# Performance work log

Measured on AMD Instinct MI355X. Metric: run time of the kernel, lower is better.

Reference implementation:

```python
import jax, jax.numpy as jnp
import numpy as np

B, S, D, H, L, FFN = 32, 512, 512, 8, 4, 1024
DH = D // H
EPS = 1e-5


def make_pe(seq, d):
    pos = np.arange(seq)[:, None].astype(np.float64)
    i = np.arange(d)[None, :]
    angle = pos / np.power(10000.0, (i // 2 * 2.0) / d)
    pe = angle.copy()
    pe[:, 0::2] = np.sin(angle[:, 0::2])
    pe[:, 1::2] = np.cos(angle[:, 1::2])
    return jnp.asarray(pe, dtype=jnp.float32)


def layer_norm(x, g, b):
    mu = jnp.mean(x, axis=-1, keepdims=True)
    var = jnp.mean((x - mu) ** 2, axis=-1, keepdims=True)
    return (x - mu) * jax.lax.rsqrt(var + EPS) * g + b


def setup_inputs() -> dict:
    key = jax.random.key(0)
    ks = jax.random.split(key, 12)
    sd = 0.02
    d = {
        "x": jax.random.normal(ks[0], (B, S, D), dtype=jnp.float32),
        "pe": make_pe(S, D),
        "Wq": jax.random.normal(ks[1], (L, D, D), dtype=jnp.float32) * sd,
        "bq": jnp.zeros((L, D), dtype=jnp.float32),
        "Wk": jax.random.normal(ks[2], (L, D, D), dtype=jnp.float32) * sd,
        "bk": jnp.zeros((L, D), dtype=jnp.float32),
        "Wv": jax.random.normal(ks[3], (L, D, D), dtype=jnp.float32) * sd,
        "bv": jnp.zeros((L, D), dtype=jnp.float32),
        "Wo": jax.random.normal(ks[4], (L, D, D), dtype=jnp.float32) * sd,
        "bo": jnp.zeros((L, D), dtype=jnp.float32),
        "ln1_g": jnp.ones((L, D), dtype=jnp.float32),
        "ln1_b": jnp.zeros((L, D), dtype=jnp.float32),
        "W1": jax.random.normal(ks[5], (L, D, FFN), dtype=jnp.float32) * sd,
        "b1": jnp.zeros((L, FFN), dtype=jnp.float32),
        "W2": jax.random.normal(ks[6], (L, FFN, D), dtype=jnp.float32) * sd,
        "b2": jnp.zeros((L, D), dtype=jnp.float32),
        "ln2_g": jnp.ones((L, D), dtype=jnp.float32),
        "ln2_b": jnp.zeros((L, D), dtype=jnp.float32),
    }
    return d


def reference(x, pe, Wq, bq, Wk, bk, Wv, bv, Wo, bo, ln1_g, ln1_b,
              W1, b1, W2, b2, ln2_g, ln2_b):
    out = x + pe  # positional encoding (dropout = identity in eval)
    scale = DH ** (-0.5)
    for l in range(L):
        # projections (B,S,D)
        Q = out @ Wq[l] + bq[l]
        K = out @ Wk[l] + bk[l]
        V = out @ Wv[l] + bv[l]
        # faithful raw view (no head transpose), matching torch .view semantics
        Qh = Q.reshape(B * H, S, DH)
        Kh = K.reshape(B * H, S, DH)
        Vh = V.reshape(B * H, S, DH)
        att = jnp.einsum('bqd,bkd->bqk', Qh, Kh) * scale  # (B*H,S,S)
        att = jax.nn.softmax(att, axis=-1)
        ctx = jnp.einsum('bqk,bkd->bqd', att, Vh).reshape(B, S, D)
        a = layer_norm(ctx @ Wo[l] + bo[l] + out, ln1_g[l], ln1_b[l])
        # position-wise FFN
        h = jax.nn.relu(a @ W1[l] + b1[l])
        out = layer_norm(h @ W2[l] + b2[l] + a, ln2_g[l], ln2_b[l])
    return out.reshape(B, S * D)
```

## Files before the change

### kernel.cpp

```cpp
#include <hip/hip_runtime.h>
#include <stdint.h>

#define NB 32
#define NS 512
#define ND 512
#define NH 8
#define NL 4
#define NF 1024
#define NDH 64
#define NM (NB*NS)
#define WLSTRIDE 2097152

typedef __attribute__((ext_vector_type(8))) short bf16x8;
typedef __attribute__((ext_vector_type(4))) float f32x4;

__device__ __forceinline__ short f2bf(float f) {
    union { float f; uint32_t u; } v; v.f = f;
    uint32_t r = (v.u + 0x7FFFu + ((v.u >> 16) & 1u)) >> 16;
    return (short)r;
}
__device__ __forceinline__ float bf2f(short s) {
    union { uint32_t u; float f; } v; v.u = ((uint32_t)(uint16_t)s) << 16;
    return v.f;
}
__device__ __forceinline__ f32x4 mfma16(bf16x8 a, bf16x8 b, f32x4 c) {
    return __builtin_amdgcn_mfma_f32_16x16x32_bf16(a, b, c, 0, 0, 0);
}
__device__ __forceinline__ void gld16(const void* g, void* l) {
    __builtin_amdgcn_global_load_lds(
        (const __attribute__((address_space(1))) void*)g,
        (__attribute__((address_space(3))) void*)l, 16, 0, 0);
}
__device__ __forceinline__ void xcd_swz(int& bx, int& by, int gx, int gy) {
    int n = gx * gy;
    int f = by * gx + bx;
    int q = n >> 3;
    int xcd = f & 7, idx = f >> 3;
    int s = xcd * q + idx;
    bx = s % gx; by = s / gx;
}

__global__ __launch_bounds__(256) void convT_k(const float* __restrict__ src,
        short* __restrict__ dst, int K, int N, int woff, int total)
{
    int i = blockIdx.x * 256 + threadIdx.x;
    if (i >= total) return;
    int per = K * N;
    int l = i / per, r = i - l * per;
    int n = r / K, k = r - n * K;
    dst[(size_t)l * WLSTRIDE + woff + r] = f2bf(src[(size_t)l * per + (size_t)k * N + n]);
}

__global__ __launch_bounds__(256) void biaspack_k(const float* __restrict__ bq,
        const float* __restrict__ bk, const float* __restrict__ bv, float* __restrict__ out)
{
    int i = blockIdx.x * 256 + threadIdx.x;
    if (i >= NL * 1536) return;
    int l = i / 1536, j = i - l * 1536;
    float v = (j < 512) ? bq[l * 512 + j] : (j < 1024) ? bk[l * 512 + j - 512]
                                                       : bv[l * 512 + j - 1024];
    out[i] = v;
}

__global__ __launch_bounds__(256) void addpe_k(const float* __restrict__ x,
        const float* __restrict__ pe, short* __restrict__ X)
{
    size_t i = ((size_t)blockIdx.x * 256 + threadIdx.x) * 8;
    size_t sd = i % (size_t)(NS * ND);
    f32x4 a0 = *(const f32x4*)(x + i);
    f32x4 a1 = *(const f32x4*)(x + i + 4);
    f32x4 p0 = *(const f32x4*)(pe + sd);
    f32x4 p1 = *(const f32x4*)(pe + sd + 4);
    bf16x8 r;
    #pragma unroll
    for (int j = 0; j < 4; j++) { r[j] = f2bf(a0[j] + p0[j]); r[4 + j] = f2bf(a1[j] + p1[j]); }
    *(bf16x8*)(X + i) = r;
}

template<int EPI>
__global__ __launch_bounds__(256) void gemm_bt(
        const short* __restrict__ A, const short* __restrict__ Bt,
        const float* __restrict__ bias, const short* __restrict__ res,
        void* __restrict__ C0, void* __restrict__ C1, void* __restrict__ C2,
        int M, int N, int K)
{
    __shared__ __align__(16) short Al[8192];
    __shared__ __align__(16) short Bl[8192];
    const int tid = threadIdx.x;
    const int wid = tid >> 6, lane = tid & 63;
    int bx = blockIdx.x, by = blockIdx.y;
    xcd_swz(bx, by, gridDim.x, gridDim.y);
    const int m0 = by * 128, n0 = bx * 128;
    const int wr = wid >> 1, wc = wid & 1;

    f32x4 acc[4][4];
    f32x4 zz = {0.f, 0.f, 0.f, 0.f};
    #pragma unroll
    for (int i = 0; i < 4; i++)
        #pragma unroll
        for (int j = 0; j < 4; j++) acc[i][j] = zz;

    const size_t rk = (size_t)K * 2;
    const char* Ab = (const char*)A + (size_t)m0 * rk;
    const char* Bb = (const char*)Bt + (size_t)n0 * rk;

    int srow[4], scol[4];
    #pragma unroll
    for (int c = 0; c < 4; c++) {
        int p = c * 4096 + tid * 16;
        int l = p ^ (((p >> 7) & 7) << 4);
        srow[c] = l >> 7;  scol[c] = l & 127;
    }

    for (int k0 = 0; k0 < K; k0 += 64) {
        __syncthreads();
        #pragma unroll
        for (int c = 0; c < 4; c++)
            gld16(Ab + (size_t)srow[c] * rk + (size_t)k0 * 2 + scol[c],
                  (char*)Al + c * 4096 + wid * 1024);
        #pragma unroll
        for (int c = 0; c < 4; c++)
            gld16(Bb + (size_t)srow[c] * rk + (size_t)k0 * 2 + scol[c],
                  (char*)Bl + c * 4096 + wid * 1024);
        __syncthreads();
        #pragma unroll
        for (int ks = 0; ks < 2; ks++) {
            bf16x8 af[4], bfr[4];
            #pragma unroll
            for (int mf = 0; mf < 4; mf++) {
                int row = wr * 64 + mf * 16 + (lane & 15);
                int off = (row * 128 + ks * 64 + ((lane >> 4) * 16)) ^ ((row & 7) << 4);
                af[mf] = *(const bf16x8*)((const char*)Al + off);
            }
            #pragma unroll
            for (int nf = 0; nf < 4; nf++) {
                int row = wc * 64 + nf * 16 + (lane & 15);
                int off = (row * 128 + ks * 64 + ((lane >> 4) * 16)) ^ ((row & 7) << 4);
                bfr[nf] = *(const bf16x8*)((const char*)Bl + off);
            }
            #pragma unroll
            for (int mf = 0; mf < 4; mf++)
                #pragma unroll
                for (int nf = 0; nf < 4; nf++)
                    acc[mf][nf] = mfma16(af[mf], bfr[nf], acc[mf][nf]);
        }
    }

    void* outp;
    int colbase, ostride;
    if (EPI == 0) {
        int seg = n0 >> 9;
        outp = (seg == 0) ? C0 : (seg == 1) ? C1 : C2;
        colbase = n0 & 511; ostride = 512;
    } else {
        outp = C0; colbase = n0; ostride = N;
    }

    #pragma unroll
    for (int mf = 0; mf < 4; mf++) {
        #pragma unroll
        for (int nf = 0; nf < 4; nf++) {
            int colg = n0 + wc * 64 + nf * 16 + (lane & 15);
            int col  = colbase + wc * 64 + nf * 16 + (lane & 15);
            float bi = bias[colg];
            #pragma unroll
            for (int r = 0; r < 4; r++) {
                int row = m0 + wr * 64 + mf * 16 + ((lane >> 4) << 2) + r;
                float v = acc[mf][nf][r] + bi;
                if (EPI == 0) {
                    ((short*)outp)[(size_t)row * 512 + col] = f2bf(v);
                } else if (EPI == 1) {
                    ((short*)outp)[(size_t)row * ostride + col] = f2bf(fmaxf(v, 0.f));
                } else {
                    v += bf2f(res[(size_t)row * ostride + col]);
                    ((float*)outp)[(size_t)row * ostride + col] = v;
                }
            }
        }
    }
}

__global__ __launch_bounds__(256) void vtrans_k(const short* __restrict__ V,
        short* __restrict__ VT)
{
    __shared__ short T[64][65];
    const int tid = threadIdx.x;
    const int r0 = blockIdx.x * 64, g = blockIdx.y;
    const size_t base = (size_t)g * 32768;
    #pragma unroll
    for (int rep = 0; rep < 2; rep++) {
        int chunk = rep * 256 + tid;
        int sr = chunk >> 3, c8 = (chunk & 7) * 8;
        bf16x8 v = *(const bf16x8*)(V + base + (size_t)(r0 + sr) * 64 + c8);
        #pragma unroll
        for (int j = 0; j < 8; j++) T[sr][c8 + j] = v[j];
    }
    __syncthreads();
    #pragma unroll
    for (int rep = 0; rep < 2; rep++) {
        int chunk = rep * 256 + tid;
        int dh = chunk >> 3, c8 = (chunk & 7) * 8;
        bf16x8 w;
        #pragma unroll
        for (int j = 0; j < 8; j++) w[j] = T[c8 + j][dh];
        *(bf16x8*)(VT + base + (size_t)dh * 512 + r0 + c8) = w;
    }
}

__global__ __launch_bounds__(256) void attn_k(
        const short* __restrict__ Q, const short* __restrict__ Kb,
        const short* __restrict__ VT, short* __restrict__ ctx)
{
    __shared__ __align__(16) short Kl[4096];
    __shared__ __align__(16) short Vl[4096];
    __shared__ __align__(16) short Pl[8192];
    const int tid = threadIdx.x, wid = tid >> 6, lane = tid & 63;
    int bx = blockIdx.x, by = blockIdx.y;
    xcd_swz(bx, by, gridDim.x, gridDim.y);
    const int g = by, q0 = bx * 128;
    const size_t base = (size_t)g * 32768;
    const float C = 0.18033688f;

    bf16x8 qa[2][2];
    #pragma unroll
    for (int qf = 0; qf < 2; qf++)
        #pragma unroll
        for (int ks = 0; ks < 2; ks++)
            qa[qf][ks] = *(const bf16x8*)(Q + base
                + (size_t)(q0 + wid * 32 + qf * 16 + (lane & 15)) * 64
                + ks * 32 + ((lane >> 4) * 8));

    f32x4 o[2][4];
    float ps[2][4];
    f32x4 zz = {0.f, 0.f, 0.f, 0.f};
    #pragma unroll
    for (int qf = 0; qf < 2; qf++) {
        #pragma unroll
        for (int nf = 0; nf < 4; nf++) o[qf][nf] = zz;
        #pragma unroll
        for (int r = 0; r < 4; r++) ps[qf][r] = 0.f;
    }

    const char* Kbase = (const char*)(Kb + base);
    const char* Vbase = (const char*)(VT + base);

    int srow[2], scol[2];
    #pragma unroll
    for (int c = 0; c < 2; c++) {
        int p = c * 4096 + tid * 16;
        int l = p ^ (((p >> 7) & 7) << 4);
        srow[c] = l >> 7;  scol[c] = l & 127;
    }

    for (int kt = 0; kt < 8; kt++) {
        __syncthreads();
        #pragma unroll
        for (int c = 0; c < 2; c++) {
            int p = c * 4096 + tid * 16;
            int sp = p ^ (((p >> 7) & 7) << 4);
            gld16(Kbase + (size_t)kt * 8192 + sp, (char*)Kl + c * 4096 + wid * 1024);
        }
        #pragma unroll
        for (int c = 0; c < 2; c++)
            gld16(Vbase + (size_t)srow[c] * 1024 + kt * 128 + scol[c],
                  (char*)Vl + c * 4096 + wid * 1024);
        __syncthreads();

        f32x4 sc[2][4];
        #pragma unroll
        for (int qf = 0; qf < 2; qf++)
            #pragma unroll
            for (int nf = 0; nf < 4; nf++) sc[qf][nf] = zz;
        #pragma unroll
        for (int ks = 0; ks < 2; ks++) {
            #pragma unroll
            for (int nf = 0; nf < 4; nf++) {
                int kvr = nf * 16 + (lane & 15);
                int bo = (kvr * 128 + ks * 64 + ((lane >> 4) * 16)) ^ ((kvr & 7) << 4);
                bf16x8 kf = *(const bf16x8*)((const char*)Kl + bo);
                #pragma unroll
                for (int qf = 0; qf < 2; qf++)
                    sc[qf][nf] = mfma16(qa[qf][ks], kf, sc[qf][nf]);
            }
        }

        #pragma unroll
        for (int qf = 0; qf < 2; qf++) {
            #pragma unroll
            for (int r = 0; r < 4; r++) {
                int qr = wid * 32 + qf * 16 + ((lane >> 4) << 2) + r;
                float s4 = 0.f;
                #pragma unroll
                for (int nf = 0; nf < 4; nf++) {
                    float p = __builtin_amdgcn_exp2f(sc[qf][nf][r] * C);
                    s4 += p;
                    int bo = (qr * 128 + (nf * 16 + (lane & 15)) * 2) ^ ((qr & 7) << 4);
                    *(short*)((char*)Pl + bo) = f2bf(p);
                }
                ps[qf][r] += s4;
            }
        }

        #pragma unroll
        for (int ks = 0; ks < 2; ks++) {
            bf16x8 pa[2];
            #pragma unroll
            for (int qf = 0; qf < 2; qf++) {
                int qrb = wid * 32 + qf * 16 + (lane & 15);
                int bo = (qrb * 128 + ks * 64 + ((lane >> 4) * 16)) ^ ((qrb & 7) << 4);
                pa[qf] = *(const bf16x8*)((const char*)Pl + bo);
            }
            #pragma unroll
            for (int nf = 0; nf < 4; nf++) {
                int dh = nf * 16 + (lane & 15);
                int bo2 = (dh * 128 + ks * 64 + ((lane >> 4) * 16)) ^ ((dh & 7) << 4);
                bf16x8 vf = *(const bf16x8*)((const char*)Vl + bo2);
                #pragma unroll
                for (int qf = 0; qf < 2; qf++)
                    o[qf][nf] = mfma16(pa[qf], vf, o[qf][nf]);
            }
        }
    }

    #pragma unroll
    for (int qf = 0; qf < 2; qf++) {
        #pragma unroll
        for (int r = 0; r < 4; r++) {
            float s = ps[qf][r];
            s += __shfl_xor(s, 1);
            s += __shfl_xor(s, 2);
            s += __shfl_xor(s, 4);
            s += __shfl_xor(s, 8);
            float inv = 1.f / s;
            int qr = q0 + wid * 32 + qf * 16 + ((lane >> 4) << 2) + r;
            #pragma unroll
            for (int nf = 0; nf < 4; nf++) {
                int dh = nf * 16 + (lane & 15);
                ctx[base + (size_t)qr * 64 + dh] = f2bf(o[qf][nf][r] * inv);
            }
        }
    }
}

template<int OUTF32>
__global__ __launch_bounds__(256) void ln_k(
        const float* __restrict__ pre, const float* __restrict__ g,
        const float* __restrict__ b, void* __restrict__ out)
{
    int row = blockIdx.x * 4 + (threadIdx.x >> 6);
    int lane = threadIdx.x & 63;
    const float* x = pre + (size_t)row * ND + lane * 8;
    f32x4 a0 = *(const f32x4*)x;
    f32x4 a1 = *(const f32x4*)(x + 4);
    float s = 0.f, sq = 0.f;
    #pragma unroll
    for (int j = 0; j < 4; j++) { s += a0[j]; sq += a0[j] * a0[j]; s += a1[j]; sq += a1[j] * a1[j]; }
    #pragma unroll
    for (int d = 1; d < 64; d <<= 1) { s += __shfl_xor(s, d); sq += __shfl_xor(sq, d); }
    float mean = s * (1.f / ND);
    float var = sq * (1.f / ND) - mean * mean;
    float rstd = rsqrtf(var + 1e-5f);
    const float* gp = g + lane * 8;
    const float* bp = b + lane * 8;
    if (OUTF32) {
        float* op = (float*)out + (size_t)row * ND + lane * 8;
        f32x4 r0, r1;
        #pragma unroll
        for (int j = 0; j < 4; j++) {
            r0[j] = (a0[j] - mean) * rstd * gp[j] + bp[j];
            r1[j] = (a1[j] - mean) * rstd * gp[4 + j] + bp[4 + j];
        }
        *(f32x4*)op = r0;
        *(f32x4*)(op + 4) = r1;
    } else {
        bf16x8 rr;
        #pragma unroll
        for (int j = 0; j < 4; j++) {
            rr[j]     = f2bf((a0[j] - mean) * rstd * gp[j] + bp[j]);
            rr[4 + j] = f2bf((a1[j] - mean) * rstd * gp[4 + j] + bp[4 + j]);
        }
        *(bf16x8*)((short*)out + (size_t)row * ND + lane * 8) = rr;
    }
}

extern "C" void kernel_launch(void* const* d_in, const int* in_sizes, int n_in,
                              void* d_out, int out_size, void* d_ws, size_t ws_size,
                              hipStream_t stream)
{
    (void)in_sizes; (void)n_in; (void)out_size; (void)ws_size;
    const float* x   = (const float*)d_in[0];
    const float* pe  = (const float*)d_in[1];
    const float* Wq  = (const float*)d_in[2];
    const float* bq  = (const float*)d_in[3];
    const float* Wk  = (const float*)d_in[4];
    const float* bk  = (const float*)d_in[5];
    const float* Wv  = (const float*)d_in[6];
    const float* bv  = (const float*)d_in[7];
    const float* Wo  = (const float*)d_in[8];
    const float* bo  = (const float*)d_in[9];
    const float* g1  = (const float*)d_in[10];
    const float* be1 = (const float*)d_in[11];
    const float* W1  = (const float*)d_in[12];
    const float* b1  = (const float*)d_in[13];
    const float* W2  = (const float*)d_in[14];
    const float* b2  = (const float*)d_in[15];
    const float* g2  = (const float*)d_in[16];
    const float* be2 = (const float*)d_in[17];

    char* ws = (char*)d_ws;
    const size_t MB = 1048576;
    short* WT   = (short*)(ws);
    short* XB   = (short*)(ws + 16 * MB);
    short* QB   = (short*)(ws + 32 * MB);
    short* KB   = (short*)(ws + 48 * MB);
    short* VB   = (short*)(ws + 64 * MB);
    short* VTb  = (short*)(ws + 80 * MB);
    short* CT   = (short*)(ws + 96 * MB);
    float* BQKV = (float*)(ws + 112 * MB);
    short* AB   = QB;
    float* PR   = (float*)KB;
    short* HB   = VTb;

    convT_k<<<dim3((NL*ND*ND + 255) / 256), 256, 0, stream>>>(Wq, WT, ND, ND, 0,       NL*ND*ND);
    convT_k<<<dim3((NL*ND*ND + 255) / 256), 256, 0, stream>>>(Wk, WT, ND, ND, 262144,  NL*ND*ND);
    convT_k<<<dim3((NL*ND*ND + 255) / 256), 256, 0, stream>>>(Wv, WT, ND, ND, 524288,  NL*ND*ND);
    convT_k<<<dim3((NL*ND*ND + 255) / 256), 256, 0, stream>>>(Wo, WT, ND, ND, 786432,  NL*ND*ND);
    convT_k<<<dim3((NL*ND*NF + 255) / 256), 256, 0, stream>>>(W1, WT, ND, NF, 1048576, NL*ND*NF);
    convT_k<<<dim3((NL*NF*ND + 255) / 256), 256, 0, stream>>>(W2, WT, NF, ND, 1572864, NL*NF*ND);
    biaspack_k<<<dim3(24), 256, 0, stream>>>(bq, bk, bv, BQKV);

    addpe_k<<<dim3(4096), 256, 0, stream>>>(x, pe, XB);

    for (int l = 0; l < NL; l++) {
        const short* wl = WT + (size_t)l * WLSTRIDE;
        gemm_bt<0><<<dim3(12, 128), 256, 0, stream>>>(XB, wl, BQKV + l*1536, nullptr,
                                                      QB, KB, VB, NM, 1536, ND);
        vtrans_k<<<dim3(8, 256), 256, 0, stream>>>(VB, VTb);
        attn_k<<<dim3(4, 256), 256, 0, stream>>>(QB, KB, VTb, CT);
        gemm_bt<2><<<dim3(4, 128), 256, 0, stream>>>(CT, wl + 786432, bo + l*ND, XB,
                                                     PR, nullptr, nullptr, NM, ND, ND);
        ln_k<0><<<dim3(4096), 256, 0, stream>>>(PR, g1 + l*ND, be1 + l*ND, AB);
        gemm_bt<1><<<dim3(8, 128), 256, 0, stream>>>(AB, wl + 1048576, b1 + l*NF, nullptr,
                                                     HB, nullptr, nullptr, NM, NF, ND);
        gemm_bt<2><<<dim3(4, 128), 256, 0, stream>>>(HB, wl + 1572864, b2 + l*ND, AB,
                                                     PR, nullptr, nullptr, NM, ND, NF);
        if (l < NL - 1)
            ln_k<0><<<dim3(4096), 256, 0, stream>>>(PR, g2 + l*ND, be2 + l*ND, XB);
        else
            ln_k<1><<<dim3(4096), 256, 0, stream>>>(PR, g2 + l*ND, be2 + l*ND, (float*)d_out);
    }
}
```

Measured before the change: 908.1 us.

## Double-buffer LDS tiles in GEMM and attention; tile the weight transpose

The GEMM and attention kernels now keep two shared-memory buffers and issue the global-to-LDS loads for the next K tile while the current tile is being computed. Waits use explicit vmcnt counts and barriers in place of the earlier per-iteration syncthreads, so load latency is meant to hide behind MFMA work. The weight conversion/transpose kernel becomes a 64x64 LDS-tiled transpose with coalesced reads and writes. The cost is twice the LDS per block, which can lower occupancy, and the hand-written waitcnt and barrier scheme depends on each thread issuing a fixed number of loads.

Result: faster. 780.6 us (-14.0%).

```diff
diff --git a/kernel.cpp b/kernel.cpp
--- a/kernel.cpp
+++ b/kernel.cpp
@@ -12,7 +12,14 @@
 #define WLSTRIDE 2097152
 
 typedef __attribute__((ext_vector_type(8))) short bf16x8;
+typedef __attribute__((ext_vector_type(4))) short s16x4;
 typedef __attribute__((ext_vector_type(4))) float f32x4;
+
+#define VM0  asm volatile("s_waitcnt vmcnt(0)" ::: "memory")
+#define VM4  asm volatile("s_waitcnt vmcnt(4)" ::: "memory")
+#define VM8  asm volatile("s_waitcnt vmcnt(8)" ::: "memory")
+#define SCHB __builtin_amdgcn_sched_barrier(0)
+#define SB   __builtin_amdgcn_s_barrier()
 
 __device__ __forceinline__ short f2bf(float f) {
     union { float f; uint32_t u; } v; v.f = f;
@@ -41,14 +48,32 @@
 }
 
 __global__ __launch_bounds__(256) void convT_k(const float* __restrict__ src,
-        short* __restrict__ dst, int K, int N, int woff, int total)
-{
-    int i = blockIdx.x * 256 + threadIdx.x;
-    if (i >= total) return;
-    int per = K * N;
-    int l = i / per, r = i - l * per;
-    int n = r / K, k = r - n * K;
-    dst[(size_t)l * WLSTRIDE + woff + r] = f2bf(src[(size_t)l * per + (size_t)k * N + n]);
+        short* __restrict__ dst, int K, int N, int woff)
+{
+    __shared__ float T[64][65];
+    int tk = K >> 6, tn = N >> 6;
+    int bid = blockIdx.x;
+    int l = bid / (tk * tn), rb = bid % (tk * tn);
+    int k0 = (rb / tn) << 6, n0 = (rb % tn) << 6;
+    const float* s = src + (size_t)l * K * N;
+    short* d = dst + (size_t)l * WLSTRIDE + woff;
+    int tr = threadIdx.x >> 4, tc = threadIdx.x & 15;
+    #pragma unroll
+    for (int p = 0; p < 4; p++) {
+        int row = p * 16 + tr;
+        f32x4 v = *(const f32x4*)(s + (size_t)(k0 + row) * N + n0 + tc * 4);
+        #pragma unroll
+        for (int j = 0; j < 4; j++) T[row][tc * 4 + j] = v[j];
+    }
+    __syncthreads();
+    #pragma unroll
+    for (int p = 0; p < 4; p++) {
+        int nrow = p * 16 + tr;
+        s16x4 w;
+        #pragma unroll
+        for (int j = 0; j < 4; j++) w[j] = f2bf(T[tc * 4 + j][nrow]);
+        *(s16x4*)(d + (size_t)(n0 + nrow) * K + k0 + tc * 4) = w;
+    }
 }
 
 __global__ __launch_bounds__(256) void biaspack_k(const float* __restrict__ bq,
@@ -84,8 +109,8 @@
         void* __restrict__ C0, void* __restrict__ C1, void* __restrict__ C2,
         int M, int N, int K)
 {
-    __shared__ __align__(16) short Al[8192];
-    __shared__ __align__(16) short Bl[8192];
+    __shared__ __align__(16) short Al[16384];
+    __shared__ __align__(16) short Bl[16384];
     const int tid = threadIdx.x;
     const int wid = tid >> 6, lane = tid & 63;
     int bx = blockIdx.x, by = blockIdx.y;
@@ -112,17 +137,18 @@
         srow[c] = l >> 7;  scol[c] = l & 127;
     }
 
-    for (int k0 = 0; k0 < K; k0 += 64) {
-        __syncthreads();
+    auto stage = [&](int dofs, int kt) {
+        size_t kb = (size_t)(kt << 6) * 2;
         #pragma unroll
         for (int c = 0; c < 4; c++)
-            gld16(Ab + (size_t)srow[c] * rk + (size_t)k0 * 2 + scol[c],
-                  (char*)Al + c * 4096 + wid * 1024);
+            gld16(Ab + (size_t)srow[c] * rk + kb + scol[c],
+                  (char*)Al + dofs + c * 4096 + wid * 1024);
         #pragma unroll
         for (int c = 0; c < 4; c++)
-            gld16(Bb + (size_t)srow[c] * rk + (size_t)k0 * 2 + scol[c],
-                  (char*)Bl + c * 4096 + wid * 1024);
-        __syncthreads();
+            gld16(Bb + (size_t)srow[c] * rk + kb + scol[c],
+                  (char*)Bl + dofs + c * 4096 + wid * 1024);
+    };
+    auto compute = [&](int dofs) {
         #pragma unroll
         for (int ks = 0; ks < 2; ks++) {
             bf16x8 af[4], bfr[4];
@@ -130,13 +156,13 @@
             for (int mf = 0; mf < 4; mf++) {
                 int row = wr * 64 + mf * 16 + (lane & 15);
                 int off = (row * 128 + ks * 64 + ((lane >> 4) * 16)) ^ ((row & 7) << 4);
-                af[mf] = *(const bf16x8*)((const char*)Al + off);
+                af[mf] = *(const bf16x8*)((const char*)Al + dofs + off);
             }
             #pragma unroll
             for (int nf = 0; nf < 4; nf++) {
                 int row = wc * 64 + nf * 16 + (lane & 15);
                 int off = (row * 128 + ks * 64 + ((lane >> 4) * 16)) ^ ((row & 7) << 4);
-                bfr[nf] = *(const bf16x8*)((const char*)Bl + off);
+                bfr[nf] = *(const bf16x8*)((const char*)Bl + dofs + off);
             }
             #pragma unroll
             for (int mf = 0; mf < 4; mf++)
@@ -144,6 +170,21 @@
                 for (int nf = 0; nf < 4; nf++)
                     acc[mf][nf] = mfma16(af[mf], bfr[nf], acc[mf][nf]);
         }
+    };
+
+    const int nt = K >> 6;
+    stage(0, 0);
+    stage(16384, 1);
+    VM8; SCHB; SB;
+    for (int t = 0; t < nt; t += 2) {
+        compute(0);
+        SB;
+        if (t + 2 < nt) { stage(0, t + 2); VM8; } else VM0;
+        SCHB; SB;
+        compute(16384);
+        SB;
+        if (t + 3 < nt) { stage(16384, t + 3); VM8; } else VM0;
+        SCHB; SB;
     }
 
     void* outp;
@@ -211,8 +252,8 @@
         const short* __restrict__ Q, const short* __restrict__ Kb,
         const short* __restrict__ VT, short* __restrict__ ctx)
 {
-    __shared__ __align__(16) short Kl[4096];
-    __shared__ __align__(16) short Vl[4096];
+    __shared__ __align__(16) short Kl[8192];
+    __shared__ __align__(16) short Vl[8192];
     __shared__ __align__(16) short Pl[8192];
     const int tid = threadIdx.x, wid = tid >> 6, lane = tid & 63;
     int bx = blockIdx.x, by = blockIdx.y;
@@ -244,28 +285,26 @@
     const char* Kbase = (const char*)(Kb + base);
     const char* Vbase = (const char*)(VT + base);
 
-    int srow[2], scol[2];
+    int ksp[2], srow[2], scol[2];
     #pragma unroll
     for (int c = 0; c < 2; c++) {
         int p = c * 4096 + tid * 16;
-        int l = p ^ (((p >> 7) & 7) << 4);
-        srow[c] = l >> 7;  scol[c] = l & 127;
-    }
-
-    for (int kt = 0; kt < 8; kt++) {
-        __syncthreads();
-        #pragma unroll
-        for (int c = 0; c < 2; c++) {
-            int p = c * 4096 + tid * 16;
-            int sp = p ^ (((p >> 7) & 7) << 4);
-            gld16(Kbase + (size_t)kt * 8192 + sp, (char*)Kl + c * 4096 + wid * 1024);
-        }
+        ksp[c] = p ^ (((p >> 7) & 7) << 4);
+        srow[c] = ksp[c] >> 7;  scol[c] = ksp[c] & 127;
+    }
+
+    auto stage = [&](int dofs, int kt) {
+        #pragma unroll
+        for (int c = 0; c < 2; c++)
+            gld16(Kbase + (size_t)kt * 8192 + ksp[c],
+                  (char*)Kl + dofs + c * 4096 + wid * 1024);
         #pragma unroll
         for (int c = 0; c < 2; c++)
             gld16(Vbase + (size_t)srow[c] * 1024 + kt * 128 + scol[c],
-                  (char*)Vl + c * 4096 + wid * 1024);
-        __syncthreads();
-
+                  (char*)Vl + dofs + c * 4096 + wid * 1024);
+    };
+
+    auto tile = [&](int dofs) {
         f32x4 sc[2][4];
         #pragma unroll
         for (int qf = 0; qf < 2; qf++)
@@ -276,14 +315,13 @@
             #pragma unroll
             for (int nf = 0; nf < 4; nf++) {
                 int kvr = nf * 16 + (lane & 15);
-                int bo = (kvr * 128 + ks * 64 + ((lane >> 4) * 16)) ^ ((kvr & 7) << 4);
+                int bo = ((kvr * 128 + ks * 64 + ((lane >> 4) * 16)) ^ ((kvr & 7) << 4)) + dofs;
                 bf16x8 kf = *(const bf16x8*)((const char*)Kl + bo);
                 #pragma unroll
                 for (int qf = 0; qf < 2; qf++)
                     sc[qf][nf] = mfma16(qa[qf][ks], kf, sc[qf][nf]);
             }
         }
-
         #pragma unroll
         for (int qf = 0; qf < 2; qf++) {
             #pragma unroll
@@ -300,7 +338,6 @@
                 ps[qf][r] += s4;
             }
         }
-
         #pragma unroll
         for (int ks = 0; ks < 2; ks++) {
             bf16x8 pa[2];
@@ -313,13 +350,27 @@
             #pragma unroll
             for (int nf = 0; nf < 4; nf++) {
                 int dh = nf * 16 + (lane & 15);
-                int bo2 = (dh * 128 + ks * 64 + ((lane >> 4) * 16)) ^ ((dh & 7) << 4);
+                int bo2 = ((dh * 128 + ks * 64 + ((lane >> 4) * 16)) ^ ((dh & 7) << 4)) + dofs;
                 bf16x8 vf = *(const bf16x8*)((const char*)Vl + bo2);
                 #pragma unroll
                 for (int qf = 0; qf < 2; qf++)
                     o[qf][nf] = mfma16(pa[qf], vf, o[qf][nf]);
             }
         }
+    };
+
+    stage(0, 0);
+    stage(8192, 1);
+    VM4; SCHB; SB;
+    for (int kt = 0; kt < 8; kt += 2) {
+        tile(0);
+        SB;
+        if (kt + 2 < 8) { stage(0, kt + 2); VM4; } else VM0;
+        SCHB; SB;
+        tile(8192);
+        SB;
+        if (kt + 3 < 8) { stage(8192, kt + 3); VM4; } else VM0;
+        SCHB; SB;
     }
 
     #pragma unroll
@@ -421,12 +472,12 @@
     float* PR   = (float*)KB;
     short* HB   = VTb;
 
-    convT_k<<<dim3((NL*ND*ND + 255) / 256), 256, 0, stream>>>(Wq, WT, ND, ND, 0,       NL*ND*ND);
-    convT_k<<<dim3((NL*ND*ND + 255) / 256), 256, 0, stream>>>(Wk, WT, ND, ND, 262144,  NL*ND*ND);
-    convT_k<<<dim3((NL*ND*ND + 255) / 256), 256, 0, stream>>>(Wv, WT, ND, ND, 524288,  NL*ND*ND);
-    convT_k<<<dim3((NL*ND*ND + 255) / 256), 256, 0, stream>>>(Wo, WT, ND, ND, 786432,  NL*ND*ND);
-    convT_k<<<dim3((NL*ND*NF + 255) / 256), 256, 0, stream>>>(W1, WT, ND, NF, 1048576, NL*ND*NF);
-    convT_k<<<dim3((NL*NF*ND + 255) / 256), 256, 0, stream>>>(W2, WT, NF, ND, 1572864, NL*NF*ND);
+    convT_k<<<dim3(NL*8*8),  256, 0, stream>>>(Wq, WT, ND, ND, 0);
+    convT_k<<<dim3(NL*8*8),  256, 0, stream>>>(Wk, WT, ND, ND, 262144);
+    convT_k<<<dim3(NL*8*8),  256, 0, stream>>>(Wv, WT, ND, ND, 524288);
+    convT_k<<<dim3(NL*8*8),  256, 0, stream>>>(Wo, WT, ND, ND, 786432);
+    convT_k<<<dim3(NL*8*16), 256, 0, stream>>>(W1, WT, ND, NF, 1048576);
+    convT_k<<<dim3(NL*16*8), 256, 0, stream>>>(W2, WT, NF, ND, 1572864);
     biaspack_k<<<dim3(24), 256, 0, stream>>>(bq, bk, bv, BQKV);
 
     addpe_k<<<dim3(4096), 256, 0, stream>>>(x, pe, XB);
```
